# Optimization experiments

Hardware: AMD Instinct MI355X
Metric: run time of the kernel (lower is better)

Reference implementation:

```python
import jax, jax.numpy as jnp
import numpy as np

WS = 8
NH = 8
EPS = 1e-5

def layer_norm(x, g, b):
    m = jnp.mean(x, axis=-1, keepdims=True)
    v = jnp.mean(jnp.square(x - m), axis=-1, keepdims=True)
    return (x - m) * jax.lax.rsqrt(v + EPS) * g + b

def setup_inputs() -> dict:
    key = jax.random.key(0)
    ks = jax.random.split(key, 12)
    C = 512
    s = 1.0 / np.sqrt(C)
    return {
        "x": jax.random.normal(ks[0], (16, C, 96, 96), dtype=jnp.float32),
        "Wqkv": jax.random.normal(ks[1], (C, 3 * C), dtype=jnp.float32) * s,
        "bqkv": jnp.zeros((3 * C,), dtype=jnp.float32),
        "Wo": jax.random.normal(ks[2], (C, C), dtype=jnp.float32) * s,
        "bo": jnp.zeros((C,), dtype=jnp.float32),
        "g1": jnp.ones((C,), dtype=jnp.float32),
        "beta1": jnp.zeros((C,), dtype=jnp.float32),
        "W1": jax.random.normal(ks[3], (C, C), dtype=jnp.float32) * s,
        "bf1": jnp.zeros((C,), dtype=jnp.float32),
        "W2": jax.random.normal(ks[4], (C, C), dtype=jnp.float32) * s,
        "bf2": jnp.zeros((C,), dtype=jnp.float32),
        "g2": jnp.ones((C,), dtype=jnp.float32),
        "beta2": jnp.zeros((C,), dtype=jnp.float32),
    }

def _block(t, Wqkv, bqkv, Wo, bo, g1, beta1, W1, bf1, W2, bf2, g2, beta2):
    # t: [N, L, C]  (windows of L = ws*ws tokens)
    N, L, C = t.shape
    dh = C // NH
    qkv = t @ Wqkv + bqkv                       # [N, L, 3C]
    q, k, v = jnp.split(qkv, 3, axis=-1)
    q = q.reshape(N, L, NH, dh).transpose(0, 2, 1, 3)  # [N,H,L,dh]
    k = k.reshape(N, L, NH, dh).transpose(0, 2, 1, 3)
    v = v.reshape(N, L, NH, dh).transpose(0, 2, 1, 3)
    scores = jnp.einsum('nhqd,nhkd->nhqk', q, k) / jnp.sqrt(jnp.float32(dh))
    attn = jax.nn.softmax(scores, axis=-1)
    o = jnp.einsum('nhqk,nhkd->nhqd', attn, v)  # [N,H,L,dh]
    o = o.transpose(0, 2, 1, 3).reshape(N, L, C) @ Wo + bo
    x1 = layer_norm(t + o, g1, beta1)
    f = jax.nn.relu(x1 @ W1 + bf1) @ W2 + bf2
    return layer_norm(x1 + f, g2, beta2)

def reference(x, Wqkv, bqkv, Wo, bo, g1, beta1, W1, bf1, W2, bf2, g2, beta2):
    B, C, H, W = x.shape
    ws = WS
    # H, W divisible by ws (pad amounts are 0 for chosen shapes)
    nh, nw = H // ws, W // ws
    xw = x.reshape(B, C, nh, ws, nw, ws)
    xw = xw.transpose(0, 2, 4, 3, 5, 1).reshape(B * nh * nw, ws * ws, C)
    y = _block(xw, Wqkv, bqkv, Wo, bo, g1, beta1, W1, bf1, W2, bf2, g2, beta2)
    y = y.reshape(B, nh, nw, ws, ws, C)
    y = y.transpose(0, 5, 1, 3, 2, 4).reshape(B, C, H, W)
    return y
```

## Files before the change

### kernel.cpp

```cpp
#include <hip/hip_runtime.h>

typedef short short8 __attribute__((ext_vector_type(8)));
typedef float f32x4 __attribute__((ext_vector_type(4)));

#define NWIN 2304
#define CP 520
#define LP2 136
#define VTP 72
#define SMEM_BYTES 124416

static __device__ __forceinline__ unsigned short f2bf(float f) {
  unsigned int u = __float_as_uint(f);
  u += 0x7FFFu + ((u >> 16) & 1u);
  return (unsigned short)(u >> 16);
}
static __device__ __forceinline__ float bf2f(unsigned short s) {
  return __uint_as_float(((unsigned int)s) << 16);
}
static __device__ __forceinline__ f32x4 mfma16(short8 a, short8 b, f32x4 c) {
  return __builtin_amdgcn_mfma_f32_16x16x32_bf16(a, b, c, 0, 0, 0);
}
static __device__ __forceinline__ short8 lds8(const unsigned short* p) {
  return *reinterpret_cast<const short8*>(p);
}

__global__ void transpose_cvt_kernel(const float* __restrict__ in,
                                     unsigned short* __restrict__ out,
                                     int K, int N) {
  __shared__ float tile[32][33];
  int bn = blockIdx.x * 32, bk = blockIdx.y * 32;
  int tx = threadIdx.x & 31, ty = threadIdx.x >> 5;
#pragma unroll
  for (int r = 0; r < 32; r += 8)
    tile[ty + r][tx] = in[(size_t)(bk + ty + r) * N + bn + tx];
  __syncthreads();
#pragma unroll
  for (int r = 0; r < 32; r += 8)
    out[(size_t)(bn + ty + r) * K + bk + tx] = f2bf(tile[tx][ty + r]);
}

__global__ __launch_bounds__(512, 2)
void swin_fused(const float* __restrict__ x,
                const unsigned short* __restrict__ WqkvT,
                const float* __restrict__ bqkv,
                const unsigned short* __restrict__ WoT,
                const float* __restrict__ bo,
                const float* __restrict__ g1, const float* __restrict__ beta1,
                const unsigned short* __restrict__ W1T,
                const float* __restrict__ bf1,
                const unsigned short* __restrict__ W2T,
                const float* __restrict__ bf2,
                const float* __restrict__ g2, const float* __restrict__ beta2,
                float* __restrict__ out) {
  extern __shared__ unsigned char smem[];
  unsigned short* sT  = (unsigned short*)smem;
  unsigned short* sQ  = (unsigned short*)(smem + 66560);
  unsigned short* sK  = (unsigned short*)(smem + 83968);
  unsigned short* sVt = (unsigned short*)(smem + 101376);
  unsigned short* sH  = sK;
  float* sSum  = (float*)(smem + 119808);
  float* sSq   = (float*)(smem + 121856);
  float* sMean = (float*)(smem + 123904);
  float* sRstd = (float*)(smem + 124160);

  const int tid = threadIdx.x;
  const int wvid = tid >> 6, lane = tid & 63;
  const int l16 = lane & 15, lg = lane >> 4;

  const int wid = (blockIdx.x & 7) * 288 + (blockIdx.x >> 3);
  const int b = wid / 144, rem = wid % 144;
  const int h0 = (rem / 12) * 8, w0 = (rem % 12) * 8;
  const float* xb = x + (size_t)b * 512 * 9216 + (size_t)h0 * 96 + w0;
  float* ob = out + (size_t)b * 512 * 9216 + (size_t)h0 * 96 + w0;

  const int c2 = wvid * 16 + l16;
  const int hh = wvid >> 2;
  const int mt4 = wvid & 3;
  const int ycol0 = wvid * 64;

#pragma unroll
  for (int it = 0; it < 16; ++it) {
    int gid = it * 512 + tid;
    int c = gid >> 4, hr = (gid >> 1) & 7, wq = gid & 1;
    float4 v = *reinterpret_cast<const float4*>(xb + (size_t)c * 9216 + hr * 96 + wq * 4);
    int tok = hr * 8 + wq * 4;
    sT[(tok + 0) * CP + c] = f2bf(v.x);
    sT[(tok + 1) * CP + c] = f2bf(v.y);
    sT[(tok + 2) * CP + c] = f2bf(v.z);
    sT[(tok + 3) * CP + c] = f2bf(v.w);
  }
  __syncthreads();

  f32x4 Yacc[4][4] = {};

  for (int hp = 0; hp < 4; ++hp) {
    {
      const unsigned short* bq = WqkvT + (size_t)(hp * 128 + c2) * 512;
      const unsigned short* bk = bq + (size_t)512 * 512;
      const unsigned short* bv = bq + (size_t)1024 * 512;
      f32x4 acc[3][4] = {};
      short8 qw[4], kw[4], vw[4];
#pragma unroll
      for (int p = 0; p < 4; ++p) {
        int ko = p * 32 + lg * 8;
        qw[p] = *(const short8*)(bq + ko);
        kw[p] = *(const short8*)(bk + ko);
        vw[p] = *(const short8*)(bv + ko);
      }
#pragma unroll
      for (int ks = 0; ks < 16; ++ks) {
        const int ko = ks * 32 + lg * 8;
        short8 cq = qw[ks & 3], ck = kw[ks & 3], cv = vw[ks & 3];
        if (ks < 12) {
          int ko2 = (ks + 4) * 32 + lg * 8;
          qw[ks & 3] = *(const short8*)(bq + ko2);
          kw[ks & 3] = *(const short8*)(bk + ko2);
          vw[ks & 3] = *(const short8*)(bv + ko2);
        }
        short8 a0 = lds8(&sT[(l16) * CP + ko]);
        short8 a1 = lds8(&sT[(16 + l16) * CP + ko]);
        short8 a2 = lds8(&sT[(32 + l16) * CP + ko]);
        short8 a3 = lds8(&sT[(48 + l16) * CP + ko]);
        acc[0][0] = mfma16(a0, cq, acc[0][0]);
        acc[0][1] = mfma16(a1, cq, acc[0][1]);
        acc[0][2] = mfma16(a2, cq, acc[0][2]);
        acc[0][3] = mfma16(a3, cq, acc[0][3]);
        acc[1][0] = mfma16(a0, ck, acc[1][0]);
        acc[1][1] = mfma16(a1, ck, acc[1][1]);
        acc[1][2] = mfma16(a2, ck, acc[1][2]);
        acc[1][3] = mfma16(a3, ck, acc[1][3]);
        acc[2][0] = mfma16(a0, cv, acc[2][0]);
        acc[2][1] = mfma16(a1, cv, acc[2][1]);
        acc[2][2] = mfma16(a2, cv, acc[2][2]);
        acc[2][3] = mfma16(a3, cv, acc[2][3]);
      }
      const float bqv = bqkv[hp * 128 + c2];
      const float bkv = bqkv[512 + hp * 128 + c2];
      const float bvv = bqkv[1024 + hp * 128 + c2];
#pragma unroll
      for (int mt = 0; mt < 4; ++mt) {
        int tok0 = mt * 16 + lg * 4;
#pragma unroll
        for (int r = 0; r < 4; ++r) {
          sQ[(tok0 + r) * LP2 + c2] = f2bf((acc[0][mt][r] + bqv) * 0.125f);
          sK[(tok0 + r) * LP2 + c2] = f2bf(acc[1][mt][r] + bkv);
        }
        ushort4 pk;
        pk.x = f2bf(acc[2][mt][0] + bvv);
        pk.y = f2bf(acc[2][mt][1] + bvv);
        pk.z = f2bf(acc[2][mt][2] + bvv);
        pk.w = f2bf(acc[2][mt][3] + bvv);
        *reinterpret_cast<ushort4*>(&sVt[c2 * VTP + tok0]) = pk;
      }
    }
    __syncthreads();

    {
      f32x4 sc[4] = {};
#pragma unroll
      for (int ks = 0; ks < 2; ++ks) {
        int ko = hh * 64 + ks * 32 + lg * 8;
        short8 a  = lds8(&sQ[(mt4 * 16 + l16) * LP2 + ko]);
        short8 b0 = lds8(&sK[(l16) * LP2 + ko]);
        short8 b1 = lds8(&sK[(16 + l16) * LP2 + ko]);
        short8 b2 = lds8(&sK[(32 + l16) * LP2 + ko]);
        short8 b3 = lds8(&sK[(48 + l16) * LP2 + ko]);
        sc[0] = mfma16(a, b0, sc[0]);
        sc[1] = mfma16(a, b1, sc[1]);
        sc[2] = mfma16(a, b2, sc[2]);
        sc[3] = mfma16(a, b3, sc[3]);
      }
#pragma unroll
      for (int r = 0; r < 4; ++r) {
        float m = fmaxf(fmaxf(sc[0][r], sc[1][r]), fmaxf(sc[2][r], sc[3][r]));
        m = fmaxf(m, __shfl_xor(m, 1));
        m = fmaxf(m, __shfl_xor(m, 2));
        m = fmaxf(m, __shfl_xor(m, 4));
        m = fmaxf(m, __shfl_xor(m, 8));
        float e0 = __expf(sc[0][r] - m), e1 = __expf(sc[1][r] - m);
        float e2 = __expf(sc[2][r] - m), e3 = __expf(sc[3][r] - m);
        float s = e0 + e1 + e2 + e3;
        s += __shfl_xor(s, 1);
        s += __shfl_xor(s, 2);
        s += __shfl_xor(s, 4);
        s += __shfl_xor(s, 8);
        float inv = 1.0f / s;
        int row = mt4 * 16 + lg * 4 + r;
        sQ[row * LP2 + hh * 64 + l16]      = f2bf(e0 * inv);
        sQ[row * LP2 + hh * 64 + 16 + l16] = f2bf(e1 * inv);
        sQ[row * LP2 + hh * 64 + 32 + l16] = f2bf(e2 * inv);
        sQ[row * LP2 + hh * 64 + 48 + l16] = f2bf(e3 * inv);
      }
    }

    {
      f32x4 ov[4] = {};
#pragma unroll
      for (int ks = 0; ks < 2; ++ks) {
        int ko = ks * 32 + lg * 8;
        short8 a  = lds8(&sQ[(mt4 * 16 + l16) * LP2 + hh * 64 + ko]);
        short8 b0 = lds8(&sVt[(hh * 64 + l16) * VTP + ko]);
        short8 b1 = lds8(&sVt[(hh * 64 + 16 + l16) * VTP + ko]);
        short8 b2 = lds8(&sVt[(hh * 64 + 32 + l16) * VTP + ko]);
        short8 b3 = lds8(&sVt[(hh * 64 + 48 + l16) * VTP + ko]);
        ov[0] = mfma16(a, b0, ov[0]);
        ov[1] = mfma16(a, b1, ov[1]);
        ov[2] = mfma16(a, b2, ov[2]);
        ov[3] = mfma16(a, b3, ov[3]);
      }
#pragma unroll
      for (int r = 0; r < 4; ++r) {
        int row = mt4 * 16 + lg * 4 + r;
        sQ[row * LP2 + hh * 64 + l16]      = f2bf(ov[0][r]);
        sQ[row * LP2 + hh * 64 + 16 + l16] = f2bf(ov[1][r]);
        sQ[row * LP2 + hh * 64 + 32 + l16] = f2bf(ov[2][r]);
        sQ[row * LP2 + hh * 64 + 48 + l16] = f2bf(ov[3][r]);
      }
    }
    __syncthreads();

    {
      const unsigned short* wo0 = WoT + (size_t)(ycol0 + l16) * 512 + hp * 128;
      short8 wb[4][4];
#pragma unroll
      for (int ks = 0; ks < 4; ++ks)
#pragma unroll
        for (int nt = 0; nt < 4; ++nt)
          wb[ks][nt] = *(const short8*)(wo0 + (size_t)nt * 16 * 512 + ks * 32 + lg * 8);
#pragma unroll
      for (int ks = 0; ks < 4; ++ks) {
        int ko = ks * 32 + lg * 8;
        short8 a0 = lds8(&sQ[(l16) * LP2 + ko]);
        short8 a1 = lds8(&sQ[(16 + l16) * LP2 + ko]);
        short8 a2 = lds8(&sQ[(32 + l16) * LP2 + ko]);
        short8 a3 = lds8(&sQ[(48 + l16) * LP2 + ko]);
#pragma unroll
        for (int nt = 0; nt < 4; ++nt) {
          Yacc[0][nt] = mfma16(a0, wb[ks][nt], Yacc[0][nt]);
          Yacc[1][nt] = mfma16(a1, wb[ks][nt], Yacc[1][nt]);
          Yacc[2][nt] = mfma16(a2, wb[ks][nt], Yacc[2][nt]);
          Yacc[3][nt] = mfma16(a3, wb[ks][nt], Yacc[3][nt]);
        }
      }
    }
    __syncthreads();
  }

  {
#pragma unroll
    for (int nt = 0; nt < 4; ++nt) {
      int col = ycol0 + nt * 16 + l16;
      float bv = bo[col];
#pragma unroll
      for (int mt = 0; mt < 4; ++mt) {
        int row0 = mt * 16 + lg * 4;
#pragma unroll
        for (int r = 0; r < 4; ++r)
          Yacc[mt][nt][r] += bv + bf2f(sT[(row0 + r) * CP + col]);
      }
    }
#pragma unroll
    for (int mt = 0; mt < 4; ++mt) {
#pragma unroll
      for (int r = 0; r < 4; ++r) {
        float s = Yacc[mt][0][r] + Yacc[mt][1][r] + Yacc[mt][2][r] + Yacc[mt][3][r];
        float q = Yacc[mt][0][r] * Yacc[mt][0][r] + Yacc[mt][1][r] * Yacc[mt][1][r] +
                  Yacc[mt][2][r] * Yacc[mt][2][r] + Yacc[mt][3][r] * Yacc[mt][3][r];
        s += __shfl_xor(s, 1); s += __shfl_xor(s, 2);
        s += __shfl_xor(s, 4); s += __shfl_xor(s, 8);
        q += __shfl_xor(q, 1); q += __shfl_xor(q, 2);
        q += __shfl_xor(q, 4); q += __shfl_xor(q, 8);
        if (l16 == 0) {
          sSum[wvid * 64 + mt * 16 + lg * 4 + r] = s;
          sSq[wvid * 64 + mt * 16 + lg * 4 + r] = q;
        }
      }
    }
    __syncthreads();
    if (tid < 64) {
      float s = 0.f, q = 0.f;
#pragma unroll
      for (int w = 0; w < 8; ++w) { s += sSum[w * 64 + tid]; q += sSq[w * 64 + tid]; }
      float mean = s * (1.0f / 512.0f);
      float var = q * (1.0f / 512.0f) - mean * mean;
      sMean[tid] = mean;
      sRstd[tid] = rsqrtf(var + 1e-5f);
    }
    __syncthreads();
#pragma unroll
    for (int nt = 0; nt < 4; ++nt) {
      int col = ycol0 + nt * 16 + l16;
      float gv = g1[col], bv = beta1[col];
#pragma unroll
      for (int mt = 0; mt < 4; ++mt) {
        int row0 = mt * 16 + lg * 4;
#pragma unroll
        for (int r = 0; r < 4; ++r) {
          float xv = (Yacc[mt][nt][r] - sMean[row0 + r]) * sRstd[row0 + r] * gv + bv;
          sT[(row0 + r) * CP + col] = f2bf(xv);
        }
      }
    }
  }
  __syncthreads();

  f32x4 Facc[4][4] = {};
  for (int hc = 0; hc < 4; ++hc) {
    {
      const int hcol = hc * 128 + c2;
      const unsigned short* w1p = W1T + (size_t)hcol * 512;
      f32x4 u[4] = {};
      short8 wbuf[4];
#pragma unroll
      for (int p = 0; p < 4; ++p)
        wbuf[p] = *(const short8*)(w1p + p * 32 + lg * 8);
#pragma unroll
      for (int ks = 0; ks < 16; ++ks) {
        int ko = ks * 32 + lg * 8;
        short8 cw = wbuf[ks & 3];
        if (ks < 12)
          wbuf[ks & 3] = *(const short8*)(w1p + (ks + 4) * 32 + lg * 8);
        short8 a0 = lds8(&sT[(l16) * CP + ko]);
        short8 a1 = lds8(&sT[(16 + l16) * CP + ko]);
        short8 a2 = lds8(&sT[(32 + l16) * CP + ko]);
        short8 a3 = lds8(&sT[(48 + l16) * CP + ko]);
        u[0] = mfma16(a0, cw, u[0]);
        u[1] = mfma16(a1, cw, u[1]);
        u[2] = mfma16(a2, cw, u[2]);
        u[3] = mfma16(a3, cw, u[3]);
      }
      float bv = bf1[hcol];
#pragma unroll
      for (int mt = 0; mt < 4; ++mt) {
        int tok0 = mt * 16 + lg * 4;
#pragma unroll
        for (int r = 0; r < 4; ++r)
          sH[(tok0 + r) * LP2 + c2] = f2bf(fmaxf(u[mt][r] + bv, 0.0f));
      }
    }
    __syncthreads();
    {
      const unsigned short* w2p = W2T + (size_t)(ycol0 + l16) * 512 + hc * 128;
      short8 wb[4][4];
#pragma unroll
      for (int ks = 0; ks < 4; ++ks)
#pragma unroll
        for (int nt = 0; nt < 4; ++nt)
          wb[ks][nt] = *(const short8*)(w2p + (size_t)nt * 16 * 512 + ks * 32 + lg * 8);
#pragma unroll
      for (int ks = 0; ks < 4; ++ks) {
        int ko = ks * 32 + lg * 8;
        short8 a0 = lds8(&sH[(l16) * LP2 + ko]);
        short8 a1 = lds8(&sH[(16 + l16) * LP2 + ko]);
        short8 a2 = lds8(&sH[(32 + l16) * LP2 + ko]);
        short8 a3 = lds8(&sH[(48 + l16) * LP2 + ko]);
#pragma unroll
        for (int nt = 0; nt < 4; ++nt) {
          Facc[0][nt] = mfma16(a0, wb[ks][nt], Facc[0][nt]);
          Facc[1][nt] = mfma16(a1, wb[ks][nt], Facc[1][nt]);
          Facc[2][nt] = mfma16(a2, wb[ks][nt], Facc[2][nt]);
          Facc[3][nt] = mfma16(a3, wb[ks][nt], Facc[3][nt]);
        }
      }
    }
    __syncthreads();
  }

  {
#pragma unroll
    for (int nt = 0; nt < 4; ++nt) {
      int col = ycol0 + nt * 16 + l16;
      float bv = bf2[col];
#pragma unroll
      for (int mt = 0; mt < 4; ++mt) {
        int row0 = mt * 16 + lg * 4;
#pragma unroll
        for (int r = 0; r < 4; ++r)
          Facc[mt][nt][r] += bv + bf2f(sT[(row0 + r) * CP + col]);
      }
    }
#pragma unroll
    for (int mt = 0; mt < 4; ++mt) {
#pragma unroll
      for (int r = 0; r < 4; ++r) {
        float s = Facc[mt][0][r] + Facc[mt][1][r] + Facc[mt][2][r] + Facc[mt][3][r];
        float q = Facc[mt][0][r] * Facc[mt][0][r] + Facc[mt][1][r] * Facc[mt][1][r] +
                  Facc[mt][2][r] * Facc[mt][2][r] + Facc[mt][3][r] * Facc[mt][3][r];
        s += __shfl_xor(s, 1); s += __shfl_xor(s, 2);
        s += __shfl_xor(s, 4); s += __shfl_xor(s, 8);
        q += __shfl_xor(q, 1); q += __shfl_xor(q, 2);
        q += __shfl_xor(q, 4); q += __shfl_xor(q, 8);
        if (l16 == 0) {
          sSum[wvid * 64 + mt * 16 + lg * 4 + r] = s;
          sSq[wvid * 64 + mt * 16 + lg * 4 + r] = q;
        }
      }
    }
    __syncthreads();
    if (tid < 64) {
      float s = 0.f, q = 0.f;
#pragma unroll
      for (int w = 0; w < 8; ++w) { s += sSum[w * 64 + tid]; q += sSq[w * 64 + tid]; }
      float mean = s * (1.0f / 512.0f);
      float var = q * (1.0f / 512.0f) - mean * mean;
      sMean[tid] = mean;
      sRstd[tid] = rsqrtf(var + 1e-5f);
    }
    __syncthreads();
#pragma unroll
    for (int nt = 0; nt < 4; ++nt) {
      int col = ycol0 + nt * 16 + l16;
      float gv = g2[col], bv = beta2[col];
      float* op = ob + (size_t)col * 9216;
#pragma unroll
      for (int mt = 0; mt < 4; ++mt) {
        int tok0 = mt * 16 + lg * 4;
        float4 o4;
        o4.x = (Facc[mt][nt][0] - sMean[tok0 + 0]) * sRstd[tok0 + 0] * gv + bv;
        o4.y = (Facc[mt][nt][1] - sMean[tok0 + 1]) * sRstd[tok0 + 1] * gv + bv;
        o4.z = (Facc[mt][nt][2] - sMean[tok0 + 2]) * sRstd[tok0 + 2] * gv + bv;
        o4.w = (Facc[mt][nt][3] - sMean[tok0 + 3]) * sRstd[tok0 + 3] * gv + bv;
        *reinterpret_cast<float4*>(&op[(tok0 >> 3) * 96 + (tok0 & 7)]) = o4;
      }
    }
  }
}

extern "C" void kernel_launch(void* const* d_in, const int* in_sizes, int n_in,
                              void* d_out, int out_size, void* d_ws, size_t ws_size,
                              hipStream_t stream) {
  const float* x     = (const float*)d_in[0];
  const float* Wqkv  = (const float*)d_in[1];
  const float* bqkv  = (const float*)d_in[2];
  const float* Wo    = (const float*)d_in[3];
  const float* bo    = (const float*)d_in[4];
  const float* g1    = (const float*)d_in[5];
  const float* beta1 = (const float*)d_in[6];
  const float* W1    = (const float*)d_in[7];
  const float* bf1   = (const float*)d_in[8];
  const float* W2    = (const float*)d_in[9];
  const float* bf2   = (const float*)d_in[10];
  const float* g2    = (const float*)d_in[11];
  const float* beta2 = (const float*)d_in[12];
  float* out = (float*)d_out;

  unsigned short* ws = (unsigned short*)d_ws;
  unsigned short* WqkvT = ws;
  unsigned short* WoT   = ws + (size_t)1536 * 512;
  unsigned short* W1T   = WoT + (size_t)512 * 512;
  unsigned short* W2T   = W1T + (size_t)512 * 512;

  transpose_cvt_kernel<<<dim3(48, 16), 256, 0, stream>>>(Wqkv, WqkvT, 512, 1536);
  transpose_cvt_kernel<<<dim3(16, 16), 256, 0, stream>>>(Wo, WoT, 512, 512);
  transpose_cvt_kernel<<<dim3(16, 16), 256, 0, stream>>>(W1, W1T, 512, 512);
  transpose_cvt_kernel<<<dim3(16, 16), 256, 0, stream>>>(W2, W2T, 512, 512);

  (void)hipFuncSetAttribute((const void*)swin_fused,
                            hipFuncAttributeMaxDynamicSharedMemorySize, SMEM_BYTES);
  swin_fused<<<NWIN, 512, SMEM_BYTES, stream>>>(x, WqkvT, bqkv, WoT, bo, g1, beta1,
                                                W1T, bf1, W2T, bf2, g2, beta2, out);
}
```

Baseline: 1.174 ms.

## Switch projection GEMMs to 32x32x16 MFMA and XOR-swizzle LDS tiles

Replaces the 16x16x32 MFMA tiling in the QKV, output-projection and FFN GEMMs with 32x32x16 MFMA tiles, changing how the 8 waves split the 64-token by 512-channel work. Padded LDS rows become unpadded rows with an XOR swizzle on 8-element groups, which cuts LDS footprint and aims to avoid bank conflicts. The goal is fewer LDS A-operand reloads per MFMA and better weight reuse. The cost is larger per-wave accumulators, which raises register pressure at 2 blocks per CU, plus a LayerNorm reduction that now needs an extra shuffle step.

```diff
diff --git a/kernel.cpp b/kernel.cpp
--- a/kernel.cpp
+++ b/kernel.cpp
@@ -2,12 +2,10 @@
 
 typedef short short8 __attribute__((ext_vector_type(8)));
 typedef float f32x4 __attribute__((ext_vector_type(4)));
+typedef float f32x16 __attribute__((ext_vector_type(16)));
 
 #define NWIN 2304
-#define CP 520
-#define LP2 136
-#define VTP 72
-#define SMEM_BYTES 124416
+#define SMEM_BYTES 117248
 
 static __device__ __forceinline__ unsigned short f2bf(float f) {
   unsigned int u = __float_as_uint(f);
@@ -20,8 +18,20 @@
 static __device__ __forceinline__ f32x4 mfma16(short8 a, short8 b, f32x4 c) {
   return __builtin_amdgcn_mfma_f32_16x16x32_bf16(a, b, c, 0, 0, 0);
 }
+static __device__ __forceinline__ f32x16 mfma32(short8 a, short8 b, f32x16 c) {
+  return __builtin_amdgcn_mfma_f32_32x32x16_bf16(a, b, c, 0, 0, 0);
+}
 static __device__ __forceinline__ short8 lds8(const unsigned short* p) {
   return *reinterpret_cast<const short8*>(p);
+}
+static __device__ __forceinline__ int swzT(int r, int c) {
+  return r * 512 + ((((c >> 3) ^ (r & 7)) << 3) | (c & 7));
+}
+static __device__ __forceinline__ int swz128(int r, int c) {
+  return r * 128 + ((((c >> 3) ^ (r & 7)) << 3) | (c & 7));
+}
+static __device__ __forceinline__ int swzV(int r, int c) {
+  return r * 64 + ((((c >> 3) ^ (r & 7)) << 3) | (c & 7));
 }
 
 __global__ void transpose_cvt_kernel(const float* __restrict__ in,
@@ -53,19 +63,20 @@
                 const float* __restrict__ g2, const float* __restrict__ beta2,
                 float* __restrict__ out) {
   extern __shared__ unsigned char smem[];
-  unsigned short* sT  = (unsigned short*)smem;
-  unsigned short* sQ  = (unsigned short*)(smem + 66560);
-  unsigned short* sK  = (unsigned short*)(smem + 83968);
-  unsigned short* sVt = (unsigned short*)(smem + 101376);
-  unsigned short* sH  = sK;
-  float* sSum  = (float*)(smem + 119808);
-  float* sSq   = (float*)(smem + 121856);
-  float* sMean = (float*)(smem + 123904);
-  float* sRstd = (float*)(smem + 124160);
+  unsigned short* sTm  = (unsigned short*)smem;
+  unsigned short* sQm  = (unsigned short*)(smem + 65536);
+  unsigned short* sKm  = (unsigned short*)(smem + 81920);
+  unsigned short* sVtm = (unsigned short*)(smem + 98304);
+  unsigned short* sHm  = sKm;
+  float* sSum  = (float*)(smem + 114688);
+  float* sSq   = (float*)(smem + 115712);
+  float* sMean = (float*)(smem + 116736);
+  float* sRstd = (float*)(smem + 116992);
 
   const int tid = threadIdx.x;
   const int wvid = tid >> 6, lane = tid & 63;
   const int l16 = lane & 15, lg = lane >> 4;
+  const int l32 = lane & 31, kh = lane >> 5, kh8 = kh << 3;
 
   const int wid = (blockIdx.x & 7) * 288 + (blockIdx.x >> 3);
   const int b = wid / 144, rem = wid % 144;
@@ -73,10 +84,13 @@
   const float* xb = x + (size_t)b * 512 * 9216 + (size_t)h0 * 96 + w0;
   float* ob = out + (size_t)b * 512 * 9216 + (size_t)h0 * 96 + w0;
 
-  const int c2 = wvid * 16 + l16;
+  const int rt = wvid & 1;
+  const int g4 = wvid >> 1;
+  const int ctg = wvid >> 1;
   const int hh = wvid >> 2;
   const int mt4 = wvid & 3;
-  const int ycol0 = wvid * 64;
+  const int c128 = g4 * 32 + l32;
+  const int arow = rt * 32 + l32;
 
 #pragma unroll
   for (int it = 0; it < 16; ++it) {
@@ -84,73 +98,61 @@
     int c = gid >> 4, hr = (gid >> 1) & 7, wq = gid & 1;
     float4 v = *reinterpret_cast<const float4*>(xb + (size_t)c * 9216 + hr * 96 + wq * 4);
     int tok = hr * 8 + wq * 4;
-    sT[(tok + 0) * CP + c] = f2bf(v.x);
-    sT[(tok + 1) * CP + c] = f2bf(v.y);
-    sT[(tok + 2) * CP + c] = f2bf(v.z);
-    sT[(tok + 3) * CP + c] = f2bf(v.w);
+    sTm[swzT(tok + 0, c)] = f2bf(v.x);
+    sTm[swzT(tok + 1, c)] = f2bf(v.y);
+    sTm[swzT(tok + 2, c)] = f2bf(v.z);
+    sTm[swzT(tok + 3, c)] = f2bf(v.w);
   }
   __syncthreads();
 
-  f32x4 Yacc[4][4] = {};
+  f32x16 Yacc[4] = {};
 
   for (int hp = 0; hp < 4; ++hp) {
     {
-      const unsigned short* bq = WqkvT + (size_t)(hp * 128 + c2) * 512;
+      const unsigned short* bq = WqkvT + (size_t)(hp * 128 + c128) * 512;
       const unsigned short* bk = bq + (size_t)512 * 512;
       const unsigned short* bv = bq + (size_t)1024 * 512;
-      f32x4 acc[3][4] = {};
+      f32x16 aq = {}, ak = {}, av = {};
       short8 qw[4], kw[4], vw[4];
 #pragma unroll
       for (int p = 0; p < 4; ++p) {
-        int ko = p * 32 + lg * 8;
+        int ko = p * 16 + kh8;
         qw[p] = *(const short8*)(bq + ko);
         kw[p] = *(const short8*)(bk + ko);
         vw[p] = *(const short8*)(bv + ko);
       }
 #pragma unroll
-      for (int ks = 0; ks < 16; ++ks) {
-        const int ko = ks * 32 + lg * 8;
+      for (int ks = 0; ks < 32; ++ks) {
         short8 cq = qw[ks & 3], ck = kw[ks & 3], cv = vw[ks & 3];
-        if (ks < 12) {
-          int ko2 = (ks + 4) * 32 + lg * 8;
-          qw[ks & 3] = *(const short8*)(bq + ko2);
-          kw[ks & 3] = *(const short8*)(bk + ko2);
-          vw[ks & 3] = *(const short8*)(bv + ko2);
+        if (ks < 28) {
+          int ko = (ks + 4) * 16 + kh8;
+          qw[ks & 3] = *(const short8*)(bq + ko);
+          kw[ks & 3] = *(const short8*)(bk + ko);
+          vw[ks & 3] = *(const short8*)(bv + ko);
         }
-        short8 a0 = lds8(&sT[(l16) * CP + ko]);
-        short8 a1 = lds8(&sT[(16 + l16) * CP + ko]);
-        short8 a2 = lds8(&sT[(32 + l16) * CP + ko]);
-        short8 a3 = lds8(&sT[(48 + l16) * CP + ko]);
-        acc[0][0] = mfma16(a0, cq, acc[0][0]);
-        acc[0][1] = mfma16(a1, cq, acc[0][1]);
-        acc[0][2] = mfma16(a2, cq, acc[0][2]);
-        acc[0][3] = mfma16(a3, cq, acc[0][3]);
-        acc[1][0] = mfma16(a0, ck, acc[1][0]);
-        acc[1][1] = mfma16(a1, ck, acc[1][1]);
-        acc[1][2] = mfma16(a2, ck, acc[1][2]);
-        acc[1][3] = mfma16(a3, ck, acc[1][3]);
-        acc[2][0] = mfma16(a0, cv, acc[2][0]);
-        acc[2][1] = mfma16(a1, cv, acc[2][1]);
-        acc[2][2] = mfma16(a2, cv, acc[2][2]);
-        acc[2][3] = mfma16(a3, cv, acc[2][3]);
-      }
-      const float bqv = bqkv[hp * 128 + c2];
-      const float bkv = bqkv[512 + hp * 128 + c2];
-      const float bvv = bqkv[1024 + hp * 128 + c2];
-#pragma unroll
-      for (int mt = 0; mt < 4; ++mt) {
-        int tok0 = mt * 16 + lg * 4;
-#pragma unroll
-        for (int r = 0; r < 4; ++r) {
-          sQ[(tok0 + r) * LP2 + c2] = f2bf((acc[0][mt][r] + bqv) * 0.125f);
-          sK[(tok0 + r) * LP2 + c2] = f2bf(acc[1][mt][r] + bkv);
-        }
+        short8 a = lds8(sTm + swzT(arow, ks * 16 + kh8));
+        aq = mfma32(a, cq, aq);
+        ak = mfma32(a, ck, ak);
+        av = mfma32(a, cv, av);
+      }
+      const float bqv = bqkv[hp * 128 + c128];
+      const float bkv = bqkv[512 + hp * 128 + c128];
+      const float bvv = bqkv[1024 + hp * 128 + c128];
+#pragma unroll
+      for (int reg = 0; reg < 16; ++reg) {
+        int row = rt * 32 + (reg & 3) + ((reg & 12) << 1) + (kh << 2);
+        sQm[swz128(row, c128)] = f2bf((aq[reg] + bqv) * 0.125f);
+        sKm[swz128(row, c128)] = f2bf(ak[reg] + bkv);
+      }
+#pragma unroll
+      for (int q = 0; q < 4; ++q) {
+        int t0 = rt * 32 + q * 8 + (kh << 2);
         ushort4 pk;
-        pk.x = f2bf(acc[2][mt][0] + bvv);
-        pk.y = f2bf(acc[2][mt][1] + bvv);
-        pk.z = f2bf(acc[2][mt][2] + bvv);
-        pk.w = f2bf(acc[2][mt][3] + bvv);
-        *reinterpret_cast<ushort4*>(&sVt[c2 * VTP + tok0]) = pk;
+        pk.x = f2bf(av[4 * q + 0] + bvv);
+        pk.y = f2bf(av[4 * q + 1] + bvv);
+        pk.z = f2bf(av[4 * q + 2] + bvv);
+        pk.w = f2bf(av[4 * q + 3] + bvv);
+        *reinterpret_cast<ushort4*>(sVtm + swzV(c128, t0)) = pk;
       }
     }
     __syncthreads();
@@ -159,12 +161,12 @@
       f32x4 sc[4] = {};
 #pragma unroll
       for (int ks = 0; ks < 2; ++ks) {
-        int ko = hh * 64 + ks * 32 + lg * 8;
-        short8 a  = lds8(&sQ[(mt4 * 16 + l16) * LP2 + ko]);
-        short8 b0 = lds8(&sK[(l16) * LP2 + ko]);
-        short8 b1 = lds8(&sK[(16 + l16) * LP2 + ko]);
-        short8 b2 = lds8(&sK[(32 + l16) * LP2 + ko]);
-        short8 b3 = lds8(&sK[(48 + l16) * LP2 + ko]);
+        int kbase = hh * 64 + ks * 32 + lg * 8;
+        short8 a  = lds8(sQm + swz128(mt4 * 16 + l16, kbase));
+        short8 b0 = lds8(sKm + swz128(l16, kbase));
+        short8 b1 = lds8(sKm + swz128(16 + l16, kbase));
+        short8 b2 = lds8(sKm + swz128(32 + l16, kbase));
+        short8 b3 = lds8(sKm + swz128(48 + l16, kbase));
         sc[0] = mfma16(a, b0, sc[0]);
         sc[1] = mfma16(a, b1, sc[1]);
         sc[2] = mfma16(a, b2, sc[2]);
@@ -186,10 +188,10 @@
         s += __shfl_xor(s, 8);
         float inv = 1.0f / s;
         int row = mt4 * 16 + lg * 4 + r;
-        sQ[row * LP2 + hh * 64 + l16]      = f2bf(e0 * inv);
-        sQ[row * LP2 + hh * 64 + 16 + l16] = f2bf(e1 * inv);
-        sQ[row * LP2 + hh * 64 + 32 + l16] = f2bf(e2 * inv);
-        sQ[row * LP2 + hh * 64 + 48 + l16] = f2bf(e3 * inv);
+        sQm[swz128(row, hh * 64 + l16)]      = f2bf(e0 * inv);
+        sQm[swz128(row, hh * 64 + 16 + l16)] = f2bf(e1 * inv);
+        sQm[swz128(row, hh * 64 + 32 + l16)] = f2bf(e2 * inv);
+        sQm[swz128(row, hh * 64 + 48 + l16)] = f2bf(e3 * inv);
       }
     }
 
@@ -197,12 +199,12 @@
       f32x4 ov[4] = {};
 #pragma unroll
       for (int ks = 0; ks < 2; ++ks) {
-        int ko = ks * 32 + lg * 8;
-        short8 a  = lds8(&sQ[(mt4 * 16 + l16) * LP2 + hh * 64 + ko]);
-        short8 b0 = lds8(&sVt[(hh * 64 + l16) * VTP + ko]);
-        short8 b1 = lds8(&sVt[(hh * 64 + 16 + l16) * VTP + ko]);
-        short8 b2 = lds8(&sVt[(hh * 64 + 32 + l16) * VTP + ko]);
-        short8 b3 = lds8(&sVt[(hh * 64 + 48 + l16) * VTP + ko]);
+        int kbase = ks * 32 + lg * 8;
+        short8 a  = lds8(sQm + swz128(mt4 * 16 + l16, hh * 64 + kbase));
+        short8 b0 = lds8(sVtm + swzV(hh * 64 + l16, kbase));
+        short8 b1 = lds8(sVtm + swzV(hh * 64 + 16 + l16, kbase));
+        short8 b2 = lds8(sVtm + swzV(hh * 64 + 32 + l16, kbase));
+        short8 b3 = lds8(sVtm + swzV(hh * 64 + 48 + l16, kbase));
         ov[0] = mfma16(a, b0, ov[0]);
         ov[1] = mfma16(a, b1, ov[1]);
         ov[2] = mfma16(a, b2, ov[2]);
@@ -211,35 +213,33 @@
 #pragma unroll
       for (int r = 0; r < 4; ++r) {
         int row = mt4 * 16 + lg * 4 + r;
-        sQ[row * LP2 + hh * 64 + l16]      = f2bf(ov[0][r]);
-        sQ[row * LP2 + hh * 64 + 16 + l16] = f2bf(ov[1][r]);
-        sQ[row * LP2 + hh * 64 + 32 + l16] = f2bf(ov[2][r]);
-        sQ[row * LP2 + hh * 64 + 48 + l16] = f2bf(ov[3][r]);
-      }
-    }
-    __syncthreads();
-
-    {
-      const unsigned short* wo0 = WoT + (size_t)(ycol0 + l16) * 512 + hp * 128;
-      short8 wb[4][4];
-#pragma unroll
-      for (int ks = 0; ks < 4; ++ks)
-#pragma unroll
-        for (int nt = 0; nt < 4; ++nt)
-          wb[ks][nt] = *(const short8*)(wo0 + (size_t)nt * 16 * 512 + ks * 32 + lg * 8);
-#pragma unroll
-      for (int ks = 0; ks < 4; ++ks) {
-        int ko = ks * 32 + lg * 8;
-        short8 a0 = lds8(&sQ[(l16) * LP2 + ko]);
-        short8 a1 = lds8(&sQ[(16 + l16) * LP2 + ko]);
-        short8 a2 = lds8(&sQ[(32 + l16) * LP2 + ko]);
-        short8 a3 = lds8(&sQ[(48 + l16) * LP2 + ko]);
-#pragma unroll
-        for (int nt = 0; nt < 4; ++nt) {
-          Yacc[0][nt] = mfma16(a0, wb[ks][nt], Yacc[0][nt]);
-          Yacc[1][nt] = mfma16(a1, wb[ks][nt], Yacc[1][nt]);
-          Yacc[2][nt] = mfma16(a2, wb[ks][nt], Yacc[2][nt]);
-          Yacc[3][nt] = mfma16(a3, wb[ks][nt], Yacc[3][nt]);
+        sQm[swz128(row, hh * 64 + l16)]      = f2bf(ov[0][r]);
+        sQm[swz128(row, hh * 64 + 16 + l16)] = f2bf(ov[1][r]);
+        sQm[swz128(row, hh * 64 + 32 + l16)] = f2bf(ov[2][r]);
+        sQm[swz128(row, hh * 64 + 48 + l16)] = f2bf(ov[3][r]);
+      }
+    }
+    __syncthreads();
+
+    {
+      const unsigned short* wo[4];
+#pragma unroll
+      for (int ct = 0; ct < 4; ++ct)
+        wo[ct] = WoT + (size_t)(ctg * 128 + ct * 32 + l32) * 512 + hp * 128;
+      short8 wb[2][4];
+#pragma unroll
+      for (int p = 0; p < 2; ++p)
+#pragma unroll
+        for (int ct = 0; ct < 4; ++ct)
+          wb[p][ct] = *(const short8*)(wo[ct] + p * 16 + kh8);
+#pragma unroll
+      for (int ks = 0; ks < 8; ++ks) {
+        short8 a = lds8(sQm + swz128(rt * 32 + l32, ks * 16 + kh8));
+#pragma unroll
+        for (int ct = 0; ct < 4; ++ct) {
+          short8 w = wb[ks & 1][ct];
+          if (ks < 6) wb[ks & 1][ct] = *(const short8*)(wo[ct] + (ks + 2) * 16 + kh8);
+          Yacc[ct] = mfma32(a, w, Yacc[ct]);
         }
       }
     }
@@ -248,39 +248,34 @@
 
   {
 #pragma unroll
-    for (int nt = 0; nt < 4; ++nt) {
-      int col = ycol0 + nt * 16 + l16;
+    for (int ct = 0; ct < 4; ++ct) {
+      int col = ctg * 128 + ct * 32 + l32;
       float bv = bo[col];
 #pragma unroll
-      for (int mt = 0; mt < 4; ++mt) {
-        int row0 = mt * 16 + lg * 4;
-#pragma unroll
-        for (int r = 0; r < 4; ++r)
-          Yacc[mt][nt][r] += bv + bf2f(sT[(row0 + r) * CP + col]);
-      }
-    }
-#pragma unroll
-    for (int mt = 0; mt < 4; ++mt) {
-#pragma unroll
-      for (int r = 0; r < 4; ++r) {
-        float s = Yacc[mt][0][r] + Yacc[mt][1][r] + Yacc[mt][2][r] + Yacc[mt][3][r];
-        float q = Yacc[mt][0][r] * Yacc[mt][0][r] + Yacc[mt][1][r] * Yacc[mt][1][r] +
-                  Yacc[mt][2][r] * Yacc[mt][2][r] + Yacc[mt][3][r] * Yacc[mt][3][r];
-        s += __shfl_xor(s, 1); s += __shfl_xor(s, 2);
-        s += __shfl_xor(s, 4); s += __shfl_xor(s, 8);
-        q += __shfl_xor(q, 1); q += __shfl_xor(q, 2);
-        q += __shfl_xor(q, 4); q += __shfl_xor(q, 8);
-        if (l16 == 0) {
-          sSum[wvid * 64 + mt * 16 + lg * 4 + r] = s;
-          sSq[wvid * 64 + mt * 16 + lg * 4 + r] = q;
-        }
+      for (int reg = 0; reg < 16; ++reg) {
+        int row = rt * 32 + (reg & 3) + ((reg & 12) << 1) + (kh << 2);
+        Yacc[ct][reg] += bv + bf2f(sTm[swzT(row, col)]);
+      }
+    }
+#pragma unroll
+    for (int reg = 0; reg < 16; ++reg) {
+      float s = Yacc[0][reg] + Yacc[1][reg] + Yacc[2][reg] + Yacc[3][reg];
+      float q = Yacc[0][reg] * Yacc[0][reg] + Yacc[1][reg] * Yacc[1][reg] +
+                Yacc[2][reg] * Yacc[2][reg] + Yacc[3][reg] * Yacc[3][reg];
+      s += __shfl_xor(s, 1);  s += __shfl_xor(s, 2);
+      s += __shfl_xor(s, 4);  s += __shfl_xor(s, 8);  s += __shfl_xor(s, 16);
+      q += __shfl_xor(q, 1);  q += __shfl_xor(q, 2);
+      q += __shfl_xor(q, 4);  q += __shfl_xor(q, 8);  q += __shfl_xor(q, 16);
+      if (l32 == 0) {
+        int row = rt * 32 + (reg & 3) + ((reg & 12) << 1) + (kh << 2);
+        sSum[ctg * 64 + row] = s;
+        sSq[ctg * 64 + row]  = q;
       }
     }
     __syncthreads();
     if (tid < 64) {
-      float s = 0.f, q = 0.f;
-#pragma unroll
-      for (int w = 0; w < 8; ++w) { s += sSum[w * 64 + tid]; q += sSq[w * 64 + tid]; }
+      float s = sSum[tid] + sSum[64 + tid] + sSum[128 + tid] + sSum[192 + tid];
+      float q = sSq[tid] + sSq[64 + tid] + sSq[128 + tid] + sSq[192 + tid];
       float mean = s * (1.0f / 512.0f);
       float var = q * (1.0f / 512.0f) - mean * mean;
       sMean[tid] = mean;
@@ -288,78 +283,64 @@
     }
     __syncthreads();
 #pragma unroll
-    for (int nt = 0; nt < 4; ++nt) {
-      int col = ycol0 + nt * 16 + l16;
+    for (int ct = 0; ct < 4; ++ct) {
+      int col = ctg * 128 + ct * 32 + l32;
       float gv = g1[col], bv = beta1[col];
 #pragma unroll
-      for (int mt = 0; mt < 4; ++mt) {
-        int row0 = mt * 16 + lg * 4;
-#pragma unroll
-        for (int r = 0; r < 4; ++r) {
-          float xv = (Yacc[mt][nt][r] - sMean[row0 + r]) * sRstd[row0 + r] * gv + bv;
-          sT[(row0 + r) * CP + col] = f2bf(xv);
-        }
+      for (int reg = 0; reg < 16; ++reg) {
+        int row = rt * 32 + (reg & 3) + ((reg & 12) << 1) + (kh << 2);
+        float xv = (Yacc[ct][reg] - sMean[row]) * sRstd[row] * gv + bv;
+        sTm[swzT(row, col)] = f2bf(xv);
       }
     }
   }
   __syncthreads();
 
-  f32x4 Facc[4][4] = {};
+  f32x16 Facc[4] = {};
   for (int hc = 0; hc < 4; ++hc) {
     {
-      const int hcol = hc * 128 + c2;
+      const int hcol = hc * 128 + c128;
       const unsigned short* w1p = W1T + (size_t)hcol * 512;
-      f32x4 u[4] = {};
+      f32x16 u = {};
       short8 wbuf[4];
 #pragma unroll
       for (int p = 0; p < 4; ++p)
-        wbuf[p] = *(const short8*)(w1p + p * 32 + lg * 8);
-#pragma unroll
-      for (int ks = 0; ks < 16; ++ks) {
-        int ko = ks * 32 + lg * 8;
+        wbuf[p] = *(const short8*)(w1p + p * 16 + kh8);
+#pragma unroll
+      for (int ks = 0; ks < 32; ++ks) {
         short8 cw = wbuf[ks & 3];
-        if (ks < 12)
-          wbuf[ks & 3] = *(const short8*)(w1p + (ks + 4) * 32 + lg * 8);
-        short8 a0 = lds8(&sT[(l16) * CP + ko]);
-        short8 a1 = lds8(&sT[(16 + l16) * CP + ko]);
-        short8 a2 = lds8(&sT[(32 + l16) * CP + ko]);
-        short8 a3 = lds8(&sT[(48 + l16) * CP + ko]);
-        u[0] = mfma16(a0, cw, u[0]);
-        u[1] = mfma16(a1, cw, u[1]);
-        u[2] = mfma16(a2, cw, u[2]);
-        u[3] = mfma16(a3, cw, u[3]);
+        if (ks < 28)
+          wbuf[ks & 3] = *(const short8*)(w1p + (ks + 4) * 16 + kh8);
+        short8 a = lds8(sTm + swzT(arow, ks * 16 + kh8));
+        u = mfma32(a, cw, u);
       }
       float bv = bf1[hcol];
 #pragma unroll
-      for (int mt = 0; mt < 4; ++mt) {
-        int tok0 = mt * 16 + lg * 4;
-#pragma unroll
-        for (int r = 0; r < 4; ++r)
-          sH[(tok0 + r) * LP2 + c2] = f2bf(fmaxf(u[mt][r] + bv, 0.0f));
-      }
-    }
-    __syncthreads();
-    {
-      const unsigned short* w2p = W2T + (size_t)(ycol0 + l16) * 512 + hc * 128;
-      short8 wb[4][4];
-#pragma unroll
-      for (int ks = 0; ks < 4; ++ks)
-#pragma unroll
-        for (int nt = 0; nt < 4; ++nt)
-          wb[ks][nt] = *(const short8*)(w2p + (size_t)nt * 16 * 512 + ks * 32 + lg * 8);
-#pragma unroll
-      for (int ks = 0; ks < 4; ++ks) {
-        int ko = ks * 32 + lg * 8;
-        short8 a0 = lds8(&sH[(l16) * LP2 + ko]);
-        short8 a1 = lds8(&sH[(16 + l16) * LP2 + ko]);
-        short8 a2 = lds8(&sH[(32 + l16) * LP2 + ko]);
-        short8 a3 = lds8(&sH[(48 + l16) * LP2 + ko]);
-#pragma unroll
-        for (int nt = 0; nt < 4; ++nt) {
-          Facc[0][nt] = mfma16(a0, wb[ks][nt], Facc[0][nt]);
-          Facc[1][nt] = mfma16(a1, wb[ks][nt], Facc[1][nt]);
-          Facc[2][nt] = mfma16(a2, wb[ks][nt], Facc[2][nt]);
-          Facc[3][nt] = mfma16(a3, wb[ks][nt], Facc[3][nt]);
+      for (int reg = 0; reg < 16; ++reg) {
+        int row = rt * 32 + (reg & 3) + ((reg & 12) << 1) + (kh << 2);
+        sHm[swz128(row, c128)] = f2bf(fmaxf(u[reg] + bv, 0.0f));
+      }
+    }
+    __syncthreads();
+    {
+      const unsigned short* w2[4];
+#pragma unroll
+      for (int ct = 0; ct < 4; ++ct)
+        w2[ct] = W2T + (size_t)(ctg * 128 + ct * 32 + l32) * 512 + hc * 128;
+      short8 wb[2][4];
+#pragma unroll
+      for (int p = 0; p < 2; ++p)
+#pragma unroll
+        for (int ct = 0; ct < 4; ++ct)
+          wb[p][ct] = *(const short8*)(w2[ct] + p * 16 + kh8);
+#pragma unroll
+      for (int ks = 0; ks < 8; ++ks) {
+        short8 a = lds8(sHm + swz128(rt * 32 + l32, ks * 16 + kh8));
+#pragma unroll
+        for (int ct = 0; ct < 4; ++ct) {
+          short8 w = wb[ks & 1][ct];
+          if (ks < 6) wb[ks & 1][ct] = *(const short8*)(w2[ct] + (ks + 2) * 16 + kh8);
+          Facc[ct] = mfma32(a, w, Facc[ct]);
         }
       }
     }
@@ -368,39 +349,34 @@
 
   {
 #pragma unroll
-    for (int nt = 0; nt < 4; ++nt) {
-      int col = ycol0 + nt * 16 + l16;
+    for (int ct = 0; ct < 4; ++ct) {
+      int col = ctg * 128 + ct * 32 + l32;
       float bv = bf2[col];
 #pragma unroll
-      for (int mt = 0; mt < 4; ++mt) {
-        int row0 = mt * 16 + lg * 4;
-#pragma unroll
-        for (int r = 0; r < 4; ++r)
-          Facc[mt][nt][r] += bv + bf2f(sT[(row0 + r) * CP + col]);
-      }
-    }
-#pragma unroll
-    for (int mt = 0; mt < 4; ++mt) {
-#pragma unroll
-      for (int r = 0; r < 4; ++r) {
-        float s = Facc[mt][0][r] + Facc[mt][1][r] + Facc[mt][2][r] + Facc[mt][3][r];
-        float q = Facc[mt][0][r] * Facc[mt][0][r] + Facc[mt][1][r] * Facc[mt][1][r] +
-                  Facc[mt][2][r] * Facc[mt][2][r] + Facc[mt][3][r] * Facc[mt][3][r];
-        s += __shfl_xor(s, 1); s += __shfl_xor(s, 2);
-        s += __shfl_xor(s, 4); s += __shfl_xor(s, 8);
-        q += __shfl_xor(q, 1); q += __shfl_xor(q, 2);
-        q += __shfl_xor(q, 4); q += __shfl_xor(q, 8);
-        if (l16 == 0) {
-          sSum[wvid * 64 + mt * 16 + lg * 4 + r] = s;
-          sSq[wvid * 64 + mt * 16 + lg * 4 + r] = q;
-        }
+      for (int reg = 0; reg < 16; ++reg) {
+        int row = rt * 32 + (reg & 3) + ((reg & 12) << 1) + (kh << 2);
+        Facc[ct][reg] += bv + bf2f(sTm[swzT(row, col)]);
+      }
+    }
+#pragma unroll
+    for (int reg = 0; reg < 16; ++reg) {
+      float s = Facc[0][reg] + Facc[1][reg] + Facc[2][reg] + Facc[3][reg];
+      float q = Facc[0][reg] * Facc[0][reg] + Facc[1][reg] * Facc[1][reg] +
+                Facc[2][reg] * Facc[2][reg] + Facc[3][reg] * Facc[3][reg];
+      s += __shfl_xor(s, 1);  s += __shfl_xor(s, 2);
+      s += __shfl_xor(s, 4);  s += __shfl_xor(s, 8);  s += __shfl_xor(s, 16);
+      q += __shfl_xor(q, 1);  q += __shfl_xor(q, 2);
+      q += __shfl_xor(q, 4);  q += __shfl_xor(q, 8);  q += __shfl_xor(q, 16);
+      if (l32 == 0) {
+        int row = rt * 32 + (reg & 3) + ((reg & 12) << 1) + (kh << 2);
+        sSum[ctg * 64 + row] = s;
+        sSq[ctg * 64 + row]  = q;
       }
     }
     __syncthreads();
     if (tid < 64) {
-      float s = 0.f, q = 0.f;
-#pragma unroll
-      for (int w = 0; w < 8; ++w) { s += sSum[w * 64 + tid]; q += sSq[w * 64 + tid]; }
+      float s = sSum[tid] + sSum[64 + tid] + sSum[128 + tid] + sSum[192 + tid];
+      float q = sSq[tid] + sSq[64 + tid] + sSq[128 + tid] + sSq[192 + tid];
       float mean = s * (1.0f / 512.0f);
       float var = q * (1.0f / 512.0f) - mean * mean;
       sMean[tid] = mean;
@@ -408,19 +384,19 @@
     }
     __syncthreads();
 #pragma unroll
-    for (int nt = 0; nt < 4; ++nt) {
-      int col = ycol0 + nt * 16 + l16;
+    for (int ct = 0; ct < 4; ++ct) {
+      int col = ctg * 128 + ct * 32 + l32;
       float gv = g2[col], bv = beta2[col];
       float* op = ob + (size_t)col * 9216;
 #pragma unroll
-      for (int mt = 0; mt < 4; ++mt) {
-        int tok0 = mt * 16 + lg * 4;
+      for (int q4 = 0; q4 < 4; ++q4) {
+        int t0 = rt * 32 + q4 * 8 + (kh << 2);
         float4 o4;
-        o4.x = (Facc[mt][nt][0] - sMean[tok0 + 0]) * sRstd[tok0 + 0] * gv + bv;
-        o4.y = (Facc[mt][nt][1] - sMean[tok0 + 1]) * sRstd[tok0 + 1] * gv + bv;
-        o4.z = (Facc[mt][nt][2] - sMean[tok0 + 2]) * sRstd[tok0 + 2] * gv + bv;
-        o4.w = (Facc[mt][nt][3] - sMean[tok0 + 3]) * sRstd[tok0 + 3] * gv + bv;
-        *reinterpret_cast<float4*>(&op[(tok0 >> 3) * 96 + (tok0 & 7)]) = o4;
+        o4.x = (Facc[ct][4 * q4 + 0] - sMean[t0 + 0]) * sRstd[t0 + 0] * gv + bv;
+        o4.y = (Facc[ct][4 * q4 + 1] - sMean[t0 + 1]) * sRstd[t0 + 1] * gv + bv;
+        o4.z = (Facc[ct][4 * q4 + 2] - sMean[t0 + 2]) * sRstd[t0 + 2] * gv + bv;
+        o4.w = (Facc[ct][4 * q4 + 3] - sMean[t0 + 3]) * sRstd[t0 + 3] * gv + bv;
+        *reinterpret_cast<float4*>(op + (t0 >> 3) * 96 + (t0 & 7)) = o4;
       }
     }
   }
```

New measurement: 2.062 ms. +75.6%, slower.
